# Kernel tuning notes

Hardware: AMD Instinct MI355X
Metric: run time of the kernel (lower is better)

The kernel has to match this reference:

```python
import jax, jax.numpy as jnp
import numpy as np

NEG_INF = -1e30  # stands in for float('-inf'); avoids nan in masked softmax edge cases


def setup_inputs() -> dict:
    key = jax.random.key(0)
    ks = jax.random.split(key, 6)
    B, N, MD, QD, AD = 64, 512, 1024, 1024, 1024
    stdv_m = 1.0 / np.sqrt(MD)
    stdv_q = 1.0 / np.sqrt(QD)
    stdv_a = 1.0 / np.sqrt(AD)
    return {
        "memory_values": jax.random.normal(ks[0], (B, N, MD), dtype=jnp.float32),
        "mask": jax.random.randint(ks[1], (B, N), 0, 2, dtype=jnp.int32),
        "query": jax.random.normal(ks[2], (B, QD), dtype=jnp.float32),
        "Wh": jax.random.uniform(ks[3], (MD, AD), jnp.float32, -stdv_m, stdv_m),
        "Ws": jax.random.uniform(ks[4], (QD, AD), jnp.float32, -stdv_q, stdv_q),
        "v": jax.random.uniform(ks[5], (AD, 1), jnp.float32, -stdv_a, stdv_a),
    }


def reference(memory_values, mask, query, Wh, Ws, v):
    # Et(i) = tanh(Hi*Wh + St*Ws) @ v ; At = softmax(Et) with masking
    tq = query @ Ws                                   # (B, AD)
    h = jnp.tanh(memory_values @ Wh + tq[:, None, :])  # (B, N, AD)
    logits = jnp.squeeze(h @ v, axis=-1)              # (B, N)

    maskf = mask.astype(logits.dtype)
    # no_cells[b] == 1 iff every cell in row b is masked out
    no_cells = jnp.prod(1.0 - maskf, axis=1, keepdims=True)  # (B, 1)
    suppress = jnp.where(maskf == 0, NEG_INF, 0.0)
    suppress = jnp.where(no_cells == 1.0, 0.0, suppress)
    weights = jax.nn.softmax(logits + suppress, axis=-1)
    weights = jnp.where(no_cells == 1.0, 0.0, weights)

    context = jnp.einsum("bn,bnd->bd", weights, memory_values)
    return context
```

## Files before the change

### kernel.cpp

```cpp
#include <hip/hip_runtime.h>
#include <cstdint>
#include <cstddef>

typedef float floatx4 __attribute__((ext_vector_type(4)));
typedef _Float16 half8_t __attribute__((ext_vector_type(8)));
typedef _Float16 half2_t __attribute__((ext_vector_type(2)));

#define AS1 __attribute__((address_space(1)))
#define AS3 __attribute__((address_space(3)))

__device__ __forceinline__ void glds16(const void* g, void* l) {
  __builtin_amdgcn_global_load_lds((const AS1 void*)g, (AS3 void*)l, 16, 0, 0);
}

__device__ __forceinline__ half2_t pkrtz(float a, float b) {
  return __builtin_bit_cast(half2_t, __builtin_amdgcn_cvt_pkrtz(a, b));
}

__device__ __forceinline__ float fast_tanh(float x) {
  float e2 = __expf(2.f * x);
  return 1.f - 2.f * __builtin_amdgcn_rcpf(e2 + 1.f);
}

__global__ __launch_bounds__(256) void k_prep(
    const float* __restrict__ mem, _Float16* __restrict__ memh,
    const float* __restrict__ Wh, _Float16* __restrict__ WhT,
    const float* __restrict__ q, const float* __restrict__ Ws,
    float* __restrict__ tq) {
  __shared__ float sh[64 * 65];
  const int bx = blockIdx.x;
  const int tid = threadIdx.x;
  if (bx >= 1280) {
    size_t i = (((size_t)(bx - 1280) << 8) + tid) << 3;
    floatx4 a = *(const floatx4*)(mem + i);
    floatx4 b = *(const floatx4*)(mem + i + 4);
    union { half2_t h2[4]; half8_t h8; } u;
    u.h2[0] = half2_t{(_Float16)a[0], (_Float16)a[1]};
    u.h2[1] = half2_t{(_Float16)a[2], (_Float16)a[3]};
    u.h2[2] = half2_t{(_Float16)b[0], (_Float16)b[1]};
    u.h2[3] = half2_t{(_Float16)b[2], (_Float16)b[3]};
    *(half8_t*)(memh + i) = u.h8;
  } else if (bx < 256) {
    int bb = bx;
    int n0 = (bb & 15) << 6, k0 = (bb >> 4) << 6;
    int tx = tid & 63, ty = tid >> 6;
    #pragma unroll
    for (int r = ty; r < 64; r += 4) sh[r * 65 + tx] = Wh[(size_t)(k0 + r) * 1024 + n0 + tx];
    __syncthreads();
    #pragma unroll
    for (int r = ty; r < 64; r += 4)
      WhT[(size_t)(n0 + r) * 1024 + k0 + tx] = (_Float16)sh[tx * 65 + r];
  } else {
    int bb = bx - 256;
    int d0 = (bb & 15) << 6, b = bb >> 4;
    int dl = tid & 63, kg = tid >> 6;
    float* qs = sh;
    float* red = sh + 1024;
    for (int k = tid; k < 1024; k += 256) qs[k] = q[(b << 10) + k];
    __syncthreads();
    float acc = 0.f;
    int kbase = kg << 8;
    #pragma unroll 8
    for (int k = 0; k < 256; ++k)
      acc += qs[kbase + k] * Ws[(size_t)(kbase + k) * 1024 + d0 + dl];
    red[(kg << 6) + dl] = acc;
    __syncthreads();
    if (kg == 0)
      tq[(b << 10) + d0 + dl] = red[dl] + red[64 + dl] + red[128 + dl] + red[192 + dl];
  }
}

__global__ void k0_transpose(const float* __restrict__ Wh, _Float16* __restrict__ WhT) {
  __shared__ float t[64][65];
  int k0 = blockIdx.y << 6, n0 = blockIdx.x << 6;
  int tx = threadIdx.x, ty = threadIdx.y;
  #pragma unroll
  for (int r = ty; r < 64; r += 4) t[r][tx] = Wh[(size_t)(k0 + r) * 1024 + n0 + tx];
  __syncthreads();
  #pragma unroll
  for (int r = ty; r < 64; r += 4)
    WhT[(size_t)(n0 + r) * 1024 + k0 + tx] = (_Float16)t[tx][r];
}

__global__ __launch_bounds__(256) void k1_tq(const float* __restrict__ q,
                                             const float* __restrict__ Ws,
                                             float* __restrict__ tq) {
  __shared__ float qs[1024];
  __shared__ float red[4][64];
  int b = blockIdx.y;
  int d0 = blockIdx.x << 6;
  int dl = threadIdx.x & 63, kg = threadIdx.x >> 6;
  for (int k = threadIdx.x; k < 1024; k += 256) qs[k] = q[(b << 10) + k];
  __syncthreads();
  float acc = 0.f;
  int kbase = kg << 8;
  #pragma unroll 8
  for (int k = 0; k < 256; ++k)
    acc += qs[kbase + k] * Ws[(size_t)(kbase + k) * 1024 + d0 + dl];
  red[kg][dl] = acc;
  __syncthreads();
  if (kg == 0)
    tq[(b << 10) + d0 + dl] = red[0][dl] + red[1][dl] + red[2][dl] + red[3][dl];
}

__global__ __launch_bounds__(512, 2) void k2_8ph(
    const _Float16* __restrict__ Ah, const _Float16* __restrict__ BT,
    const float* __restrict__ tq, const float* __restrict__ v,
    float* __restrict__ partials) {
  extern __shared__ char smem[];
  const int bid = blockIdx.x;
  const int wg = ((bid & 7) << 6) | (bid >> 3);
  const int mtile = wg >> 2, ntile = wg & 3;
  const int m0 = mtile << 8, n0 = ntile << 8;
  const int tid = threadIdx.x;
  const int w = tid >> 6, lane = tid & 63;
  const int wm = w >> 2, wn = w & 3, quad = lane >> 4, l15 = lane & 15;

  int aoff[2][4], boff[2][2];
  #pragma unroll
  for (int ks = 0; ks < 2; ++ks) {
    int swz = ((ks << 2) + quad) ^ (l15 & 7);
    #pragma unroll
    for (int i = 0; i < 4; ++i)
      aoff[ks][i] = (wm << 14) + (((i << 4) + l15) << 7) + (swz << 4);
    #pragma unroll
    for (int j = 0; j < 2; ++j)
      boff[ks][j] = 65536 + (wn << 12) + (((j << 4) + l15) << 7) + (swz << 4);
  }

  const int rr = tid >> 3, cc = tid & 7;
  const int r5 = rr & 31;
  int aSrc[2][2], bSrc[2][2], dA[2][2], dB[2][2];
  #pragma unroll
  for (int h = 0; h < 2; ++h)
    #pragma unroll
    for (int hm = 0; hm < 2; ++hm) {
      aSrc[h][hm] = ((m0 + (hm << 7) + (h << 6) + rr) << 10) + ((cc ^ (rr & 7)) << 3);
      dA[h][hm] = (((hm << 1) + h) << 13) + (w << 10);
    }
  #pragma unroll
  for (int ch = 0; ch < 2; ++ch)
    #pragma unroll
    for (int is = 0; is < 2; ++is) {
      int wnb = (is << 1) + (rr >> 5);
      bSrc[ch][is] = ((n0 + (wnb << 6) + (ch << 5) + r5) << 10) + ((cc ^ (r5 & 7)) << 3);
      dB[ch][is] = 65536 + (ch << 14) + (is << 13) + (w << 10);
    }

  floatx4 acc[8][4];
  #pragma unroll
  for (int i = 0; i < 8; ++i)
    #pragma unroll
    for (int j = 0; j < 4; ++j) acc[i][j] = floatx4{0.f, 0.f, 0.f, 0.f};

  half8_t af[2][4], bf[2][2][2];

#define STAGE_A(H, KST, OO)                                   \
  glds16(Ah + aSrc[H][0] + (KST), smem + (OO) + dA[H][0]);    \
  glds16(Ah + aSrc[H][1] + (KST), smem + (OO) + dA[H][1]);
#define STAGE_B(CH, KST, OO)                                  \
  glds16(BT + bSrc[CH][0] + (KST), smem + (OO) + dB[CH][0]);  \
  glds16(BT + bSrc[CH][1] + (KST), smem + (OO) + dB[CH][1]);
#define VM(N) asm volatile("s_waitcnt vmcnt(" #N ")" ::: "memory");
#define BAR __builtin_amdgcn_s_barrier();
#define LOAD_AF(CO, RHOFF)                                    \
  _Pragma("unroll")                                           \
  for (int ks_ = 0; ks_ < 2; ++ks_) {                         \
    _Pragma("unroll")                                         \
    for (int i_ = 0; i_ < 4; ++i_)                            \
      af[ks_][i_] = *(const half8_t*)(smem + (CO) + (RHOFF) + aoff[ks_][i_]); \
  }
#define LOAD_BF(CH, CO, CHOFF)                                \
  _Pragma("unroll")                                           \
  for (int ks_ = 0; ks_ < 2; ++ks_) {                         \
    _Pragma("unroll")                                         \
    for (int j_ = 0; j_ < 2; ++j_)                            \
      bf[CH][ks_][j_] = *(const half8_t*)(smem + (CO) + (CHOFF) + boff[ks_][j_]); \
  }
#define MFMAS(RH, CH)                                         \
  _Pragma("unroll")                                           \
  for (int ks_ = 0; ks_ < 2; ++ks_) {                         \
    _Pragma("unroll")                                         \
    for (int i_ = 0; i_ < 4; ++i_) {                          \
      _Pragma("unroll")                                       \
      for (int j_ = 0; j_ < 2; ++j_)                          \
        acc[(RH)*4 + i_][(CH)*2 + j_] = __builtin_amdgcn_mfma_f32_16x16x32_f16( \
            af[ks_][i_], bf[CH][ks_][j_], acc[(RH)*4 + i_][(CH)*2 + j_], 0, 0, 0); \
    }                                                         \
  }
#define PRIO_MFMA(RH, CH)                                     \
  __builtin_amdgcn_s_setprio(1);                              \
  MFMAS(RH, CH)                                               \
  __builtin_amdgcn_s_setprio(0);
#define GROUPT(CO, OO, KST)                                   \
                                              \
  LOAD_AF(CO, 0)                                              \
  LOAD_BF(0, CO, 0)                                           \
  VM(2)                                                       \
  STAGE_A(0, KST, OO)                                         \
  STAGE_B(0, KST, OO)                                         \
  BAR                                                         \
  PRIO_MFMA(0, 0)                                             \
  BAR                                                         \
                                              \
  LOAD_BF(1, CO, 16384)                                       \
  VM(4)                                                       \
  STAGE_B(1, KST, OO)                                         \
  BAR                                                         \
  PRIO_MFMA(0, 1)                                             \
  BAR                                                         \
                                              \
  LOAD_AF(CO, 8192)                                           \
  STAGE_A(1, KST, OO)                                         \
  BAR                                                         \
  PRIO_MFMA(1, 0)                                             \
  BAR                                                         \
                                              \
  VM(4)                                                       \
  BAR                                                         \
  PRIO_MFMA(1, 1)                                             \
  BAR

  STAGE_A(0, 0, 0)
  STAGE_B(0, 0, 0)
  STAGE_B(1, 0, 0)
  STAGE_A(1, 0, 0)
  VM(4)
  BAR

  #pragma unroll 1
  for (int g2 = 0; g2 < 8; ++g2) {
    const int g = g2 << 1;
    const int kst1 = (g + 1) << 6;
    const int kst2 = (g2 == 7) ? (15 << 6) : ((g + 2) << 6);
    GROUPT(0, 32768, kst1)
    GROUPT(32768, 0, kst2)
  }

#undef GROUPT
#undef PRIO_MFMA
#undef MFMAS
#undef LOAD_BF
#undef LOAD_AF
#undef BAR
#undef VM
#undef STAGE_B
#undef STAGE_A

  asm volatile("s_waitcnt vmcnt(0)" ::: "memory");

  const int b = m0 >> 9;
  const int colb = n0 + (wn << 6) + l15;
  float tqv[4], vv[4];
  #pragma unroll
  for (int jf = 0; jf < 4; ++jf) {
    int n = colb + (jf << 4);
    tqv[jf] = tq[(b << 10) + n];
    vv[jf] = v[n];
  }
  #pragma unroll
  for (int rf = 0; rf < 8; ++rf) {
    #pragma unroll
    for (int r = 0; r < 4; ++r) {
      float s = 0.f;
      #pragma unroll
      for (int jf = 0; jf < 4; ++jf) s += fast_tanh(acc[rf][jf][r] + tqv[jf]) * vv[jf];
      s += __shfl_xor(s, 1);
      s += __shfl_xor(s, 2);
      s += __shfl_xor(s, 4);
      s += __shfl_xor(s, 8);
      if (l15 == 0) {
        int m = m0 + (wm << 7) + (rf << 4) + (quad << 2) + r;
        partials[m * 16 + (ntile << 2) + wn] = s;
      }
    }
  }
}

__global__ __launch_bounds__(256, 2) void k2_gemm_h(
    const _Float16* __restrict__ Ah, const _Float16* __restrict__ BT,
    const float* __restrict__ tq, const float* __restrict__ v,
    float* __restrict__ partials) {
  __shared__ _Float16 As[128 * 32];
  __shared__ _Float16 Bs[128 * 32];
  const int bid = blockIdx.x;
  const int mtile = ((bid >> 6) << 3) | (bid & 7);
  const int nblk = (bid >> 3) & 7;
  const int m0 = mtile << 7, n0 = nblk << 7;
  const int tid = threadIdx.x;
  const int w = tid >> 6, lane = tid & 63;
  const int wm = w >> 1, wn = w & 1, quad = lane >> 4, l15 = lane & 15;

  floatx4 acc[4][4];
  #pragma unroll
  for (int i = 0; i < 4; ++i)
    #pragma unroll
    for (int j = 0; j < 4; ++j) acc[i][j] = floatx4{0.f, 0.f, 0.f, 0.f};

  const _Float16 *gA[2], *gB[2];
  _Float16 *lA[2], *lB[2];
  #pragma unroll
  for (int t = 0; t < 2; ++t) {
    int L = (t << 8) + (w << 6) + lane;
    int row = L >> 2, jj = L & 3;
    int j = (jj - row - (row >> 2)) & 3;
    gA[t] = Ah + (size_t)(m0 + row) * 1024 + (j << 3);
    gB[t] = BT + (size_t)(n0 + row) * 1024 + (j << 3);
    lA[t] = As + (t << 11) + (w << 9);
    lB[t] = Bs + (t << 11) + (w << 9);
  }

  const half8_t *aaddr[4], *baddr[4];
  #pragma unroll
  for (int i = 0; i < 4; ++i) {
    int ar = (wm << 6) + (i << 4) + l15;
    aaddr[i] = (const half8_t*)(As + (ar << 5) + (((quad + ar + (ar >> 2)) & 3) << 3));
    int br = (wn << 6) + (i << 4) + l15;
    baddr[i] = (const half8_t*)(Bs + (br << 5) + (((quad + br + (br >> 2)) & 3) << 3));
  }

  for (int k0 = 0; k0 < 1024; k0 += 32) {
    __syncthreads();
    glds16(gA[0] + k0, lA[0]);
    glds16(gA[1] + k0, lA[1]);
    glds16(gB[0] + k0, lB[0]);
    glds16(gB[1] + k0, lB[1]);
    __syncthreads();
    half8_t af[4], bfr[4];
    #pragma unroll
    for (int i = 0; i < 4; ++i) af[i] = *aaddr[i];
    #pragma unroll
    for (int j = 0; j < 4; ++j) bfr[j] = *baddr[j];
    #pragma unroll
    for (int i = 0; i < 4; ++i)
      #pragma unroll
      for (int j = 0; j < 4; ++j)
        acc[i][j] = __builtin_amdgcn_mfma_f32_16x16x32_f16(af[i], bfr[j], acc[i][j], 0, 0, 0);
  }

  const int b = m0 >> 9;
  const int colbase = n0 + (wn << 6) + l15;
  float tqv[4], vv[4];
  #pragma unroll
  for (int j = 0; j < 4; ++j) {
    int n = colbase + (j << 4);
    tqv[j] = tq[(b << 10) + n];
    vv[j] = v[n];
  }
  #pragma unroll
  for (int i = 0; i < 4; ++i) {
    #pragma unroll
    for (int r = 0; r < 4; ++r) {
      float s = 0.f;
      #pragma unroll
      for (int j = 0; j < 4; ++j) s += fast_tanh(acc[i][j][r] + tqv[j]) * vv[j];
      s += __shfl_xor(s, 1);
      s += __shfl_xor(s, 2);
      s += __shfl_xor(s, 4);
      s += __shfl_xor(s, 8);
      if (l15 == 0) {
        int m = m0 + (wm << 6) + (i << 4) + (quad << 2) + r;
        partials[m * 16 + (nblk << 1) + wn] = s;
      }
    }
  }
}

__global__ __launch_bounds__(256, 2) void k2_gemm_f32(
    const float* __restrict__ A, const _Float16* __restrict__ BT,
    const float* __restrict__ tq, const float* __restrict__ v,
    float* __restrict__ partials) {
  __shared__ float As[128 * 32];
  __shared__ _Float16 Bs[128 * 32];
  const int bid = blockIdx.x;
  const int mtile = ((bid >> 6) << 3) | (bid & 7);
  const int nblk = (bid >> 3) & 7;
  const int m0 = mtile << 7, n0 = nblk << 7;
  const int tid = threadIdx.x;
  const int w = tid >> 6, lane = tid & 63;
  const int wm = w >> 1, wn = w & 1, quad = lane >> 4, l15 = lane & 15;

  floatx4 acc[4][4];
  #pragma unroll
  for (int i = 0; i < 4; ++i)
    #pragma unroll
    for (int j = 0; j < 4; ++j) acc[i][j] = floatx4{0.f, 0.f, 0.f, 0.f};

  const float* gA[4];
  float* lA[4];
  #pragma unroll
  for (int t = 0; t < 4; ++t) {
    int L = (t << 8) + (w << 6) + lane;
    int row = L >> 3, jj = L & 7;
    int j = (jj - row) & 7;
    gA[t] = A + (size_t)(m0 + row) * 1024 + (j << 2);
    lA[t] = As + (t << 10) + (w << 8);
  }
  const _Float16* gB[2];
  _Float16* lB[2];
  #pragma unroll
  for (int t = 0; t < 2; ++t) {
    int L = (t << 8) + (w << 6) + lane;
    int row = L >> 2, jj = L & 3;
    int j = (jj - row - (row >> 2)) & 3;
    gB[t] = BT + (size_t)(n0 + row) * 1024 + (j << 3);
    lB[t] = Bs + (t << 11) + (w << 9);
  }
  const floatx4* aaddr[4][2];
  #pragma unroll
  for (int i = 0; i < 4; ++i) {
    int row = (wm << 6) + (i << 4) + l15;
    #pragma unroll
    for (int h = 0; h < 2; ++h) {
      int pos = ((quad << 1) + h + row) & 7;
      aaddr[i][h] = (const floatx4*)(As + (row << 5) + (pos << 2));
    }
  }
  const half8_t* baddr[4];
  #pragma unroll
  for (int j = 0; j < 4; ++j) {
    int row = (wn << 6) + (j << 4) + l15;
    int pos = (quad + row + (row >> 2)) & 3;
    baddr[j] = (const half8_t*)(Bs + (row << 5) + (pos << 3));
  }
  for (int k0 = 0; k0 < 1024; k0 += 32) {
    __syncthreads();
    glds16(gA[0] + k0, lA[0]);
    glds16(gA[1] + k0, lA[1]);
    glds16(gA[2] + k0, lA[2]);
    glds16(gA[3] + k0, lA[3]);
    glds16(gB[0] + k0, lB[0]);
    glds16(gB[1] + k0, lB[1]);
    __syncthreads();
    half8_t af[4], bfr[4];
    #pragma unroll
    for (int i = 0; i < 4; ++i) {
      floatx4 x = *aaddr[i][0], y = *aaddr[i][1];
      union { half2_t h2[4]; half8_t h8; } u;
      u.h2[0] = pkrtz(x[0], x[1]);
      u.h2[1] = pkrtz(x[2], x[3]);
      u.h2[2] = pkrtz(y[0], y[1]);
      u.h2[3] = pkrtz(y[2], y[3]);
      af[i] = u.h8;
    }
    #pragma unroll
    for (int j = 0; j < 4; ++j) bfr[j] = *baddr[j];
    #pragma unroll
    for (int i = 0; i < 4; ++i)
      #pragma unroll
      for (int j = 0; j < 4; ++j)
        acc[i][j] = __builtin_amdgcn_mfma_f32_16x16x32_f16(af[i], bfr[j], acc[i][j], 0, 0, 0);
  }
  const int b = m0 >> 9;
  const int colbase = n0 + (wn << 6) + l15;
  float tqv[4], vv[4];
  #pragma unroll
  for (int j = 0; j < 4; ++j) {
    int n = colbase + (j << 4);
    tqv[j] = tq[(b << 10) + n];
    vv[j] = v[n];
  }
  #pragma unroll
  for (int i = 0; i < 4; ++i) {
    #pragma unroll
    for (int r = 0; r < 4; ++r) {
      float s = 0.f;
      #pragma unroll
      for (int j = 0; j < 4; ++j) s += fast_tanh(acc[i][j][r] + tqv[j]) * vv[j];
      s += __shfl_xor(s, 1);
      s += __shfl_xor(s, 2);
      s += __shfl_xor(s, 4);
      s += __shfl_xor(s, 8);
      if (l15 == 0) {
        int m = m0 + (wm << 6) + (i << 4) + (quad << 2) + r;
        partials[m * 16 + (nblk << 1) + wn] = s;
      }
    }
  }
}

__global__ __launch_bounds__(512) void k3_softmax(const float* __restrict__ partials,
                                                  const int* __restrict__ mask,
                                                  float* __restrict__ weights) {
  int b = blockIdx.x;
  int n = threadIdx.x;
  int m = (b << 9) + n;
  float s = 0.f;
  #pragma unroll
  for (int i = 0; i < 16; ++i) s += partials[m * 16 + i];
  int mk = mask[m];
  float logit = mk ? s : -1e30f;
  __shared__ float red[8];
  float x = logit;
  #pragma unroll
  for (int off = 32; off > 0; off >>= 1) x = fmaxf(x, __shfl_xor(x, off));
  if ((n & 63) == 0) red[n >> 6] = x;
  __syncthreads();
  float mx = red[0];
  #pragma unroll
  for (int i = 1; i < 8; ++i) mx = fmaxf(mx, red[i]);
  float e = mk ? __expf(logit - mx) : 0.f;
  float ss = e;
  #pragma unroll
  for (int off = 32; off > 0; off >>= 1) ss += __shfl_xor(ss, off);
  __syncthreads();
  if ((n & 63) == 0) red[n >> 6] = ss;
  __syncthreads();
  float tot = 0.f;
  #pragma unroll
  for (int i = 0; i < 8; ++i) tot += red[i];
  weights[m] = (tot > 0.f) ? e / tot : 0.f;
}

__global__ void k4_ctx_h(const _Float16* __restrict__ memh,
                         const float* __restrict__ weights, float* __restrict__ ctxp) {
  int nc = blockIdx.x, b = blockIdx.y;
  int d = threadIdx.x << 3;
  float acc[8] = {0.f, 0.f, 0.f, 0.f, 0.f, 0.f, 0.f, 0.f};
  int nbase = nc << 5;
  for (int n = nbase; n < nbase + 32; ++n) {
    float wv = weights[(b << 9) + n];
    half8_t x = *(const half8_t*)(memh + ((size_t)((b << 9) + n) << 10) + d);
    #pragma unroll
    for (int k = 0; k < 8; ++k) acc[k] += wv * (float)x[k];
  }
  float* o = ctxp + ((size_t)((b << 4) + nc) << 10) + d;
  #pragma unroll
  for (int k = 0; k < 8; ++k) o[k] = acc[k];
}

__global__ void k5_reduce16(const float* __restrict__ ctxp, float* __restrict__ out) {
  int i = (blockIdx.x << 8) + threadIdx.x;
  int b = i >> 10, d = i & 1023;
  float s = 0.f;
  #pragma unroll
  for (int cc = 0; cc < 16; ++cc) s += ctxp[((size_t)((b << 4) + cc) << 10) + d];
  out[i] = s;
}

__global__ void k4_ctx_f32(const float* __restrict__ mem, const float* __restrict__ weights,
                           float* __restrict__ ctxp) {
  int nc = blockIdx.x, b = blockIdx.y;
  int d = threadIdx.x << 3;
  floatx4 a0 = {0.f, 0.f, 0.f, 0.f}, a1 = {0.f, 0.f, 0.f, 0.f};
  int nbase = nc << 6;
  for (int n = nbase; n < nbase + 64; ++n) {
    float wv = weights[(b << 9) + n];
    const floatx4* p = (const floatx4*)(mem + ((size_t)((b << 9) + n) << 10) + d);
    a0 += wv * p[0];
    a1 += wv * p[1];
  }
  floatx4* o = (floatx4*)(ctxp + ((size_t)((b << 3) + nc) << 10) + d);
  o[0] = a0;
  o[1] = a1;
}

__global__ void k5_reduce8(const float* __restrict__ ctxp, float* __restrict__ out) {
  int i = (blockIdx.x << 8) + threadIdx.x;
  int b = i >> 10, d = i & 1023;
  float s = 0.f;
  #pragma unroll
  for (int cc = 0; cc < 8; ++cc) s += ctxp[((size_t)((b << 3) + cc) << 10) + d];
  out[i] = s;
}

extern "C" void kernel_launch(void* const* d_in, const int* in_sizes, int n_in,
                              void* d_out, int out_size, void* d_ws, size_t ws_size,
                              hipStream_t stream) {
  const float* mem = (const float*)d_in[0];
  const int* mask = (const int*)d_in[1];
  const float* query = (const float*)d_in[2];
  const float* Wh = (const float*)d_in[3];
  const float* Ws = (const float*)d_in[4];
  const float* v = (const float*)d_in[5];
  float* out = (float*)d_out;

  char* ws = (char*)d_ws;
  const size_t need16 = (73ull << 20);

  if (ws_size >= need16) {
    _Float16* memh = (_Float16*)ws;
    _Float16* WhT = (_Float16*)(ws + (64ull << 20));
    float* partials = (float*)(ws + (66ull << 20));
    float* tq = (float*)(ws + (68ull << 20));
    float* weights = (float*)(ws + (68ull << 20) + (256 << 10));
    float* ctxp = (float*)(ws + (69ull << 20));

    static int use8 = -1;
    if (use8 < 0) {
      use8 = (hipFuncSetAttribute((const void*)k2_8ph,
                                  hipFuncAttributeMaxDynamicSharedMemorySize,
                                  131072) == hipSuccess) ? 1 : 0;
    }

    k_prep<<<17664, 256, 0, stream>>>(mem, memh, Wh, WhT, query, Ws, tq);
    if (use8)
      k2_8ph<<<512, 512, 131072, stream>>>(memh, WhT, tq, v, partials);
    else
      k2_gemm_h<<<2048, 256, 0, stream>>>(memh, WhT, tq, v, partials);
    k3_softmax<<<64, 512, 0, stream>>>(partials, mask, weights);
    k4_ctx_h<<<dim3(16, 64), 128, 0, stream>>>(memh, weights, ctxp);
    k5_reduce16<<<256, 256, 0, stream>>>(ctxp, out);
  } else {
    _Float16* WhT = (_Float16*)ws;
    float* partials = (float*)(ws + ((size_t)2 << 20));
    float* tq = (float*)(ws + ((size_t)4 << 20));
    float* weights = (float*)(ws + ((size_t)4 << 20) + (256 << 10));
    float* ctxp = (float*)(ws + ((size_t)9 << 19));

    k0_transpose<<<dim3(16, 16), dim3(64, 4), 0, stream>>>(Wh, WhT);
    k1_tq<<<dim3(16, 64), 256, 0, stream>>>(query, Ws, tq);
    k2_gemm_f32<<<2048, 256, 0, stream>>>(mem, WhT, tq, v, partials);
    k3_softmax<<<64, 512, 0, stream>>>(partials, mask, weights);
    k4_ctx_f32<<<dim3(8, 64), 128, 0, stream>>>(mem, weights, ctxp);
    k5_reduce8<<<256, 256, 0, stream>>>(ctxp, out);
  }
}
```

Measured before the change: 295.1 us.

## Fuse fp32-to-fp16 conversion of memory into the GEMM A-tile loading

```diff
diff --git a/kernel.cpp b/kernel.cpp
--- a/kernel.cpp
+++ b/kernel.cpp
@@ -23,26 +23,14 @@
 }
 
 __global__ __launch_bounds__(256) void k_prep(
-    const float* __restrict__ mem, _Float16* __restrict__ memh,
     const float* __restrict__ Wh, _Float16* __restrict__ WhT,
     const float* __restrict__ q, const float* __restrict__ Ws,
     float* __restrict__ tq) {
   __shared__ float sh[64 * 65];
   const int bx = blockIdx.x;
   const int tid = threadIdx.x;
-  if (bx >= 1280) {
-    size_t i = (((size_t)(bx - 1280) << 8) + tid) << 3;
-    floatx4 a = *(const floatx4*)(mem + i);
-    floatx4 b = *(const floatx4*)(mem + i + 4);
-    union { half2_t h2[4]; half8_t h8; } u;
-    u.h2[0] = half2_t{(_Float16)a[0], (_Float16)a[1]};
-    u.h2[1] = half2_t{(_Float16)a[2], (_Float16)a[3]};
-    u.h2[2] = half2_t{(_Float16)b[0], (_Float16)b[1]};
-    u.h2[3] = half2_t{(_Float16)b[2], (_Float16)b[3]};
-    *(half8_t*)(memh + i) = u.h8;
-  } else if (bx < 256) {
-    int bb = bx;
-    int n0 = (bb & 15) << 6, k0 = (bb >> 4) << 6;
+  if (bx < 256) {
+    int n0 = (bx & 15) << 6, k0 = (bx >> 4) << 6;
     int tx = tid & 63, ty = tid >> 6;
     #pragma unroll
     for (int r = ty; r < 64; r += 4) sh[r * 65 + tx] = Wh[(size_t)(k0 + r) * 1024 + n0 + tx];
@@ -70,41 +58,8 @@
   }
 }
 
-__global__ void k0_transpose(const float* __restrict__ Wh, _Float16* __restrict__ WhT) {
-  __shared__ float t[64][65];
-  int k0 = blockIdx.y << 6, n0 = blockIdx.x << 6;
-  int tx = threadIdx.x, ty = threadIdx.y;
-  #pragma unroll
-  for (int r = ty; r < 64; r += 4) t[r][tx] = Wh[(size_t)(k0 + r) * 1024 + n0 + tx];
-  __syncthreads();
-  #pragma unroll
-  for (int r = ty; r < 64; r += 4)
-    WhT[(size_t)(n0 + r) * 1024 + k0 + tx] = (_Float16)t[tx][r];
-}
-
-__global__ __launch_bounds__(256) void k1_tq(const float* __restrict__ q,
-                                             const float* __restrict__ Ws,
-                                             float* __restrict__ tq) {
-  __shared__ float qs[1024];
-  __shared__ float red[4][64];
-  int b = blockIdx.y;
-  int d0 = blockIdx.x << 6;
-  int dl = threadIdx.x & 63, kg = threadIdx.x >> 6;
-  for (int k = threadIdx.x; k < 1024; k += 256) qs[k] = q[(b << 10) + k];
-  __syncthreads();
-  float acc = 0.f;
-  int kbase = kg << 8;
-  #pragma unroll 8
-  for (int k = 0; k < 256; ++k)
-    acc += qs[kbase + k] * Ws[(size_t)(kbase + k) * 1024 + d0 + dl];
-  red[kg][dl] = acc;
-  __syncthreads();
-  if (kg == 0)
-    tq[(b << 10) + d0 + dl] = red[0][dl] + red[1][dl] + red[2][dl] + red[3][dl];
-}
-
 __global__ __launch_bounds__(512, 2) void k2_8ph(
-    const _Float16* __restrict__ Ah, const _Float16* __restrict__ BT,
+    const float* __restrict__ Af, const _Float16* __restrict__ BT,
     const float* __restrict__ tq, const float* __restrict__ v,
     float* __restrict__ partials) {
   extern __shared__ char smem[];
@@ -130,14 +85,13 @@
 
   const int rr = tid >> 3, cc = tid & 7;
   const int r5 = rr & 31;
-  int aSrc[2][2], bSrc[2][2], dA[2][2], dB[2][2];
-  #pragma unroll
-  for (int h = 0; h < 2; ++h)
-    #pragma unroll
-    for (int hm = 0; hm < 2; ++hm) {
-      aSrc[h][hm] = ((m0 + (hm << 7) + (h << 6) + rr) << 10) + ((cc ^ (rr & 7)) << 3);
-      dA[h][hm] = (((hm << 1) + h) << 13) + (w << 10);
-    }
+  int aSrcF[4];
+  #pragma unroll
+  for (int s = 0; s < 4; ++s)
+    aSrcF[s] = ((m0 + ((s >> 1) << 7) + ((s & 1) << 6) + rr) << 10) + ((cc ^ (rr & 7)) << 3);
+  const int awDst = tid << 4;
+
+  int bSrc[2][2], dB[2][2];
   #pragma unroll
   for (int ch = 0; ch < 2; ++ch)
     #pragma unroll
@@ -154,14 +108,30 @@
     for (int j = 0; j < 4; ++j) acc[i][j] = floatx4{0.f, 0.f, 0.f, 0.f};
 
   half8_t af[2][4], bf[2][2][2];
-
-#define STAGE_A(H, KST, OO)                                   \
-  glds16(Ah + aSrc[H][0] + (KST), smem + (OO) + dA[H][0]);    \
-  glds16(Ah + aSrc[H][1] + (KST), smem + (OO) + dA[H][1]);
+  floatx4 areg[4][2];
+
+#define ALOADS(KST)                                                \
+  _Pragma("unroll")                                                \
+  for (int s_ = 0; s_ < 4; ++s_) {                                 \
+    areg[s_][0] = *(const floatx4*)(Af + aSrcF[s_] + (KST));       \
+    areg[s_][1] = *(const floatx4*)(Af + aSrcF[s_] + (KST) + 4);   \
+  }                                                                \
+  asm volatile("" ::: "memory");
+#define AWRITE(OO)                                                 \
+  _Pragma("unroll")                                                \
+  for (int s_ = 0; s_ < 4; ++s_) {                                 \
+    union { half2_t h2[4]; half8_t h8; } u_;                       \
+    u_.h2[0] = pkrtz(areg[s_][0][0], areg[s_][0][1]);              \
+    u_.h2[1] = pkrtz(areg[s_][0][2], areg[s_][0][3]);              \
+    u_.h2[2] = pkrtz(areg[s_][1][0], areg[s_][1][1]);              \
+    u_.h2[3] = pkrtz(areg[s_][1][2], areg[s_][1][3]);              \
+    *(half8_t*)(smem + (OO) + (s_ << 13) + awDst) = u_.h8;         \
+  }
 #define STAGE_B(CH, KST, OO)                                  \
   glds16(BT + bSrc[CH][0] + (KST), smem + (OO) + dB[CH][0]);  \
   glds16(BT + bSrc[CH][1] + (KST), smem + (OO) + dB[CH][1]);
-#define VM(N) asm volatile("s_waitcnt vmcnt(" #N ")" ::: "memory");
+#define VM0 asm volatile("s_waitcnt vmcnt(0)" ::: "memory");
+#define LGKM0 asm volatile("s_waitcnt lgkmcnt(0)" ::: "memory");
 #define BAR __builtin_amdgcn_s_barrier();
 #define LOAD_AF(CO, RHOFF)                                    \
   _Pragma("unroll")                                           \
@@ -193,39 +163,39 @@
   MFMAS(RH, CH)                                               \
   __builtin_amdgcn_s_setprio(0);
 #define GROUPT(CO, OO, KST)                                   \
-                                              \
+                                                      \
   LOAD_AF(CO, 0)                                              \
   LOAD_BF(0, CO, 0)                                           \
-  VM(2)                                                       \
-  STAGE_A(0, KST, OO)                                         \
+  ALOADS(KST)                                                 \
   STAGE_B(0, KST, OO)                                         \
+  STAGE_B(1, KST, OO)                                         \
   BAR                                                         \
   PRIO_MFMA(0, 0)                                             \
   BAR                                                         \
-                                              \
+                                                      \
   LOAD_BF(1, CO, 16384)                                       \
-  VM(4)                                                       \
-  STAGE_B(1, KST, OO)                                         \
   BAR                                                         \
   PRIO_MFMA(0, 1)                                             \
   BAR                                                         \
-                                              \
+                                                      \
+  AWRITE(OO)                                                  \
   LOAD_AF(CO, 8192)                                           \
-  STAGE_A(1, KST, OO)                                         \
   BAR                                                         \
   PRIO_MFMA(1, 0)                                             \
   BAR                                                         \
-                                              \
-  VM(4)                                                       \
+                                                      \
+  LGKM0                                                       \
+  VM0                                                         \
   BAR                                                         \
   PRIO_MFMA(1, 1)                                             \
   BAR
 
-  STAGE_A(0, 0, 0)
+  ALOADS(0)
   STAGE_B(0, 0, 0)
   STAGE_B(1, 0, 0)
-  STAGE_A(1, 0, 0)
-  VM(4)
+  AWRITE(0)
+  LGKM0
+  VM0
   BAR
 
   #pragma unroll 1
@@ -243,9 +213,11 @@
 #undef LOAD_BF
 #undef LOAD_AF
 #undef BAR
-#undef VM
+#undef LGKM0
+#undef VM0
 #undef STAGE_B
-#undef STAGE_A
+#undef AWRITE
+#undef ALOADS
 
   asm volatile("s_waitcnt vmcnt(0)" ::: "memory");
 
@@ -277,11 +249,11 @@
   }
 }
 
-__global__ __launch_bounds__(256, 2) void k2_gemm_h(
-    const _Float16* __restrict__ Ah, const _Float16* __restrict__ BT,
+__global__ __launch_bounds__(256, 2) void k2_gemm_f32(
+    const float* __restrict__ A, const _Float16* __restrict__ BT,
     const float* __restrict__ tq, const float* __restrict__ v,
     float* __restrict__ partials) {
-  __shared__ _Float16 As[128 * 32];
+  __shared__ float As[128 * 32];
   __shared__ _Float16 Bs[128 * 32];
   const int bid = blockIdx.x;
   const int mtile = ((bid >> 6) << 3) | (bid & 7);
@@ -297,38 +269,63 @@
     #pragma unroll
     for (int j = 0; j < 4; ++j) acc[i][j] = floatx4{0.f, 0.f, 0.f, 0.f};
 
-  const _Float16 *gA[2], *gB[2];
-  _Float16 *lA[2], *lB[2];
+  const float* gA[4];
+  float* lA[4];
+  #pragma unroll
+  for (int t = 0; t < 4; ++t) {
+    int L = (t << 8) + (w << 6) + lane;
+    int row = L >> 3, jj = L & 7;
+    int j = (jj - row) & 7;
+    gA[t] = A + (size_t)(m0 + row) * 1024 + (j << 2);
+    lA[t] = As + (t << 10) + (w << 8);
+  }
+  const _Float16* gB[2];
+  _Float16* lB[2];
   #pragma unroll
   for (int t = 0; t < 2; ++t) {
     int L = (t << 8) + (w << 6) + lane;
     int row = L >> 2, jj = L & 3;
     int j = (jj - row - (row >> 2)) & 3;
-    gA[t] = Ah + (size_t)(m0 + row) * 1024 + (j << 3);
     gB[t] = BT + (size_t)(n0 + row) * 1024 + (j << 3);
-    lA[t] = As + (t << 11) + (w << 9);
     lB[t] = Bs + (t << 11) + (w << 9);
   }
-
-  const half8_t *aaddr[4], *baddr[4];
+  const floatx4* aaddr[4][2];
   #pragma unroll
   for (int i = 0; i < 4; ++i) {
-    int ar = (wm << 6) + (i << 4) + l15;
-    aaddr[i] = (const half8_t*)(As + (ar << 5) + (((quad + ar + (ar >> 2)) & 3) << 3));
-    int br = (wn << 6) + (i << 4) + l15;
-    baddr[i] = (const half8_t*)(Bs + (br << 5) + (((quad + br + (br >> 2)) & 3) << 3));
-  }
-
+    int row = (wm << 6) + (i << 4) + l15;
+    #pragma unroll
+    for (int h = 0; h < 2; ++h) {
+      int pos = ((quad << 1) + h + row) & 7;
+      aaddr[i][h] = (const floatx4*)(As + (row << 5) + (pos << 2));
+    }
+  }
+  const half8_t* baddr[4];
+  #pragma unroll
+  for (int j = 0; j < 4; ++j) {
+    int row = (wn << 6) + (j << 4) + l15;
+    int pos = (quad + row + (row >> 2)) & 3;
+    baddr[j] = (const half8_t*)(Bs + (row << 5) + (pos << 3));
+  }
   for (int k0 = 0; k0 < 1024; k0 += 32) {
     __syncthreads();
     glds16(gA[0] + k0, lA[0]);
     glds16(gA[1] + k0, lA[1]);
+    glds16(gA[2] + k0, lA[2]);
+    glds16(gA[3] + k0, lA[3]);
     glds16(gB[0] + k0, lB[0]);
     glds16(gB[1] + k0, lB[1]);
     __syncthreads();
     half8_t af[4], bfr[4];
     #pragma unroll
-    for (int i = 0; i < 4; ++i) af[i] = *aaddr[i];
+    for (int i = 0; i < 4; ++i) {
+      floatx4 x = *aaddr[i][0], y = *aaddr[i][1];
+      union { half2_t h2[4]; half8_t h8; } u;
+      u.h2[0] = pkrtz(x[0], x[1]);
+      u.h2[1] = pkrtz(x[2], x[3]);
+      u.h2[2] = pkrtz(y[0], y[1]);
+      u.h2[3] = pkrtz(y[2], y[3]);
+      af[i] = u.h8;
+    }
     #pragma unroll
     for (int j = 0; j < 4; ++j) bfr[j] = *baddr[j];
     #pragma unroll
@@ -337,7 +334,6 @@
       for (int j = 0; j < 4; ++j)
         acc[i][j] = __builtin_amdgcn_mfma_f32_16x16x32_f16(af[i], bfr[j], acc[i][j], 0, 0, 0);
   }
-
   const int b = m0 >> 9;
   const int colbase = n0 + (wn << 6) + l15;
   float tqv[4], vv[4];
@@ -366,119 +362,6 @@
   }
 }
 
-__global__ __launch_bounds__(256, 2) void k2_gemm_f32(
-    const float* __restrict__ A, const _Float16* __restrict__ BT,
-    const float* __restrict__ tq, const float* __restrict__ v,
-    float* __restrict__ partials) {
-  __shared__ float As[128 * 32];
-  __shared__ _Float16 Bs[128 * 32];
-  const int bid = blockIdx.x;
-  const int mtile = ((bid >> 6) << 3) | (bid & 7);
-  const int nblk = (bid >> 3) & 7;
-  const int m0 = mtile << 7, n0 = nblk << 7;
-  const int tid = threadIdx.x;
-  const int w = tid >> 6, lane = tid & 63;
-  const int wm = w >> 1, wn = w & 1, quad = lane >> 4, l15 = lane & 15;
-
-  floatx4 acc[4][4];
-  #pragma unroll
-  for (int i = 0; i < 4; ++i)
-    #pragma unroll
-    for (int j = 0; j < 4; ++j) acc[i][j] = floatx4{0.f, 0.f, 0.f, 0.f};
-
-  const float* gA[4];
-  float* lA[4];
-  #pragma unroll
-  for (int t = 0; t < 4; ++t) {
-    int L = (t << 8) + (w << 6) + lane;
-    int row = L >> 3, jj = L & 7;
-    int j = (jj - row) & 7;
-    gA[t] = A + (size_t)(m0 + row) * 1024 + (j << 2);
-    lA[t] = As + (t << 10) + (w << 8);
-  }
-  const _Float16* gB[2];
-  _Float16* lB[2];
-  #pragma unroll
-  for (int t = 0; t < 2; ++t) {
-    int L = (t << 8) + (w << 6) + lane;
-    int row = L >> 2, jj = L & 3;
-    int j = (jj - row - (row >> 2)) & 3;
-    gB[t] = BT + (size_t)(n0 + row) * 1024 + (j << 3);
-    lB[t] = Bs + (t << 11) + (w << 9);
-  }
-  const floatx4* aaddr[4][2];
-  #pragma unroll
-  for (int i = 0; i < 4; ++i) {
-    int row = (wm << 6) + (i << 4) + l15;
-    #pragma unroll
-    for (int h = 0; h < 2; ++h) {
-      int pos = ((quad << 1) + h + row) & 7;
-      aaddr[i][h] = (const floatx4*)(As + (row << 5) + (pos << 2));
-    }
-  }
-  const half8_t* baddr[4];
-  #pragma unroll
-  for (int j = 0; j < 4; ++j) {
-    int row = (wn << 6) + (j << 4) + l15;
-    int pos = (quad + row + (row >> 2)) & 3;
-    baddr[j] = (const half8_t*)(Bs + (row << 5) + (pos << 3));
-  }
-  for (int k0 = 0; k0 < 1024; k0 += 32) {
-    __syncthreads();
-    glds16(gA[0] + k0, lA[0]);
-    glds16(gA[1] + k0, lA[1]);
-    glds16(gA[2] + k0, lA[2]);
-    glds16(gA[3] + k0, lA[3]);
-    glds16(gB[0] + k0, lB[0]);
-    glds16(gB[1] + k0, lB[1]);
-    __syncthreads();
-    half8_t af[4], bfr[4];
-    #pragma unroll
-    for (int i = 0; i < 4; ++i) {
-      floatx4 x = *aaddr[i][0], y = *aaddr[i][1];
-      union { half2_t h2[4]; half8_t h8; } u;
-      u.h2[0] = pkrtz(x[0], x[1]);
-      u.h2[1] = pkrtz(x[2], x[3]);
-      u.h2[2] = pkrtz(y[0], y[1]);
-      u.h2[3] = pkrtz(y[2], y[3]);
-      af[i] = u.h8;
-    }
-    #pragma unroll
-    for (int j = 0; j < 4; ++j) bfr[j] = *baddr[j];
-    #pragma unroll
-    for (int i = 0; i < 4; ++i)
-      #pragma unroll
-      for (int j = 0; j < 4; ++j)
-        acc[i][j] = __builtin_amdgcn_mfma_f32_16x16x32_f16(af[i], bfr[j], acc[i][j], 0, 0, 0);
-  }
-  const int b = m0 >> 9;
-  const int colbase = n0 + (wn << 6) + l15;
-  float tqv[4], vv[4];
-  #pragma unroll
-  for (int j = 0; j < 4; ++j) {
-    int n = colbase + (j << 4);
-    tqv[j] = tq[(b << 10) + n];
-    vv[j] = v[n];
-  }
-  #pragma unroll
-  for (int i = 0; i < 4; ++i) {
-    #pragma unroll
-    for (int r = 0; r < 4; ++r) {
-      float s = 0.f;
-      #pragma unroll
-      for (int j = 0; j < 4; ++j) s += fast_tanh(acc[i][j][r] + tqv[j]) * vv[j];
-      s += __shfl_xor(s, 1);
-      s += __shfl_xor(s, 2);
-      s += __shfl_xor(s, 4);
-      s += __shfl_xor(s, 8);
-      if (l15 == 0) {
-        int m = m0 + (wm << 6) + (i << 4) + (quad << 2) + r;
-        partials[m * 16 + (nblk << 1) + wn] = s;
-      }
-    }
-  }
-}
-
 __global__ __launch_bounds__(512) void k3_softmax(const float* __restrict__ partials,
                                                   const int* __restrict__ mask,
                                                   float* __restrict__ weights) {
@@ -510,32 +393,6 @@
   #pragma unroll
   for (int i = 0; i < 8; ++i) tot += red[i];
   weights[m] = (tot > 0.f) ? e / tot : 0.f;
-}
-
-__global__ void k4_ctx_h(const _Float16* __restrict__ memh,
-                         const float* __restrict__ weights, float* __restrict__ ctxp) {
-  int nc = blockIdx.x, b = blockIdx.y;
-  int d = threadIdx.x << 3;
-  float acc[8] = {0.f, 0.f, 0.f, 0.f, 0.f, 0.f, 0.f, 0.f};
-  int nbase = nc << 5;
-  for (int n = nbase; n < nbase + 32; ++n) {
-    float wv = weights[(b << 9) + n];
-    half8_t x = *(const half8_t*)(memh + ((size_t)((b << 9) + n) << 10) + d);
-    #pragma unroll
-    for (int k = 0; k < 8; ++k) acc[k] += wv * (float)x[k];
-  }
-  float* o = ctxp + ((size_t)((b << 4) + nc) << 10) + d;
-  #pragma unroll
-  for (int k = 0; k < 8; ++k) o[k] = acc[k];
-}
-
-__global__ void k5_reduce16(const float* __restrict__ ctxp, float* __restrict__ out) {
-  int i = (blockIdx.x << 8) + threadIdx.x;
-  int b = i >> 10, d = i & 1023;
-  float s = 0.f;
-  #pragma unroll
-  for (int cc = 0; cc < 16; ++cc) s += ctxp[((size_t)((b << 4) + cc) << 10) + d];
-  out[i] = s;
 }
 
 __global__ void k4_ctx_f32(const float* __restrict__ mem, const float* __restrict__ weights,
@@ -576,43 +433,25 @@
   float* out = (float*)d_out;
 
   char* ws = (char*)d_ws;
-  const size_t need16 = (73ull << 20);
-
-  if (ws_size >= need16) {
-    _Float16* memh = (_Float16*)ws;
-    _Float16* WhT = (_Float16*)(ws + (64ull << 20));
-    float* partials = (float*)(ws + (66ull << 20));
-    float* tq = (float*)(ws + (68ull << 20));
-    float* weights = (float*)(ws + (68ull << 20) + (256 << 10));
-    float* ctxp = (float*)(ws + (69ull << 20));
-
-    static int use8 = -1;
-    if (use8 < 0) {
-      use8 = (hipFuncSetAttribute((const void*)k2_8ph,
-                                  hipFuncAttributeMaxDynamicSharedMemorySize,
-                                  131072) == hipSuccess) ? 1 : 0;
-    }
-
-    k_prep<<<17664, 256, 0, stream>>>(mem, memh, Wh, WhT, query, Ws, tq);
-    if (use8)
-      k2_8ph<<<512, 512, 131072, stream>>>(memh, WhT, tq, v, partials);
-    else
-      k2_gemm_h<<<2048, 256, 0, stream>>>(memh, WhT, tq, v, partials);
-    k3_softmax<<<64, 512, 0, stream>>>(partials, mask, weights);
-    k4_ctx_h<<<dim3(16, 64), 128, 0, stream>>>(memh, weights, ctxp);
-    k5_reduce16<<<256, 256, 0, stream>>>(ctxp, out);
-  } else {
-    _Float16* WhT = (_Float16*)ws;
-    float* partials = (float*)(ws + ((size_t)2 << 20));
-    float* tq = (float*)(ws + ((size_t)4 << 20));
-    float* weights = (float*)(ws + ((size_t)4 << 20) + (256 << 10));
-    float* ctxp = (float*)(ws + ((size_t)9 << 19));
-
-    k0_transpose<<<dim3(16, 16), dim3(64, 4), 0, stream>>>(Wh, WhT);
-    k1_tq<<<dim3(16, 64), 256, 0, stream>>>(query, Ws, tq);
+  _Float16* WhT = (_Float16*)ws;
+  float* partials = (float*)(ws + (2ull << 20));
+  float* tq = (float*)(ws + (4ull << 20));
+  float* weights = (float*)(ws + (4ull << 20) + (256 << 10));
+  float* ctxp = (float*)(ws + ((size_t)9 << 19));
+
+  static int use8 = -1;
+  if (use8 < 0) {
+    use8 = (hipFuncSetAttribute((const void*)k2_8ph,
+                                hipFuncAttributeMaxDynamicSharedMemorySize,
+                                131072) == hipSuccess) ? 1 : 0;
+  }
+
+  k_prep<<<1280, 256, 0, stream>>>(Wh, WhT, query, Ws, tq);
+  if (use8)
+    k2_8ph<<<512, 512, 131072, stream>>>(mem, WhT, tq, v, partials);
+  else
     k2_gemm_f32<<<2048, 256, 0, stream>>>(mem, WhT, tq, v, partials);
-    k3_softmax<<<64, 512, 0, stream>>>(partials, mask, weights);
-    k4_ctx_f32<<<dim3(8, 64), 128, 0, stream>>>(mem, weights, ctxp);
-    k5_reduce8<<<256, 256, 0, stream>>>(ctxp, out);
-  }
-}
+  k3_softmax<<<64, 512, 0, stream>>>(partials, mask, weights);
+  k4_ctx_f32<<<dim3(8, 64), 128, 0, stream>>>(mem, weights, ctxp);
+  k5_reduce8<<<256, 256, 0, stream>>>(ctxp, out);
+}
```

New measurement: 350.5 us. 1.19x slower.
